# Kernel tuning notes

Hardware: AMD Instinct MI355X
Metric: run time of the kernel (lower is better)

## Reference

```python
import jax, jax.numpy as jnp
import numpy as np

AGENT_THRESH = 0.5
X_DIS_THRESH = 1.5
Y_DIS_THRESH = 3.0
DIS_THRESH = 3.0
LOSS_WEIGHT = 1.0
BIG = 1000000.0

B, A, M, T, C = 128, 2048, 6, 12, 10


def setup_inputs() -> dict:
    key = jax.random.key(0)
    k1, k2, k3, k4, k5 = jax.random.split(key, 5)
    return {
        "ego_fut_preds": jax.random.normal(k1, (B, T, 2), dtype=jnp.float32),
        "agent_preds": jax.random.normal(k2, (B, A, 2), dtype=jnp.float32),
        "agent_fut_preds": jax.random.normal(k3, (B, A, M, T, 2), dtype=jnp.float32),
        "agent_score_preds": jax.random.uniform(k4, (B, A, C), dtype=jnp.float32),
        "agent_fut_cls_preds": jax.random.normal(k5, (B, A, M), dtype=jnp.float32),
    }


def _plan_collision_loss(ego_fut_preds, agent_preds, agent_fut_preds,
                         agent_score_preds, agent_fut_cls_preds):
    # --- invalidate low-score / non-vehicle agents -------------------------
    max_score = jnp.max(agent_score_preds, axis=-1)           # [B, A]
    max_idx = jnp.argmax(agent_score_preds, axis=-1)          # [B, A]
    invalid = (max_score < AGENT_THRESH) | (max_idx > 4)      # [B, A]
    afp = jnp.where(invalid[:, :, None, None, None], BIG, agent_fut_preds)

    # --- select best mode per agent ---------------------------------------
    best_mode = jnp.argmax(agent_fut_cls_preds, axis=-1)      # [B, A]
    afp = jnp.take_along_axis(
        afp, best_mode[:, :, None, None, None], axis=2
    ).squeeze(2)                                              # [B, A, T, 2]

    # --- cumsum deltas -> trajectories -------------------------------------
    pred = jnp.cumsum(ego_fut_preds, axis=-2)                 # [B, T, 2]
    afp = jnp.cumsum(afp, axis=-2)                            # [B, A, T, 2]
    target = agent_preds[:, :, None, :] + afp                 # [B, A, T, 2]

    # --- pairwise distances, far-agent masking -----------------------------
    diff = pred[:, None, :, :] - target                       # [B, A, T, 2]
    dist = jnp.linalg.norm(diff, axis=-1)                     # [B, A, T]
    target = jnp.where((dist > DIS_THRESH)[..., None], BIG, target)

    x_dist = jnp.abs(pred[:, None, :, 0] - target[..., 0])    # [B, A, T]
    y_dist = jnp.abs(pred[:, None, :, 1] - target[..., 1])    # [B, A, T]

    # argmin over agents then gather == min over agents
    x_min = jnp.min(x_dist, axis=1)                           # [B, T]
    y_min = jnp.min(y_dist, axis=1)                           # [B, T]

    x_loss = jnp.where(x_min > X_DIS_THRESH, 0.0, X_DIS_THRESH - x_min)
    y_loss = jnp.where(y_min > Y_DIS_THRESH, 0.0, Y_DIS_THRESH - y_min)
    loss = jnp.stack([x_loss, y_loss], axis=-1)               # [B, T, 2]

    # reduction='mean', weight=None, avg_factor=None
    return LOSS_WEIGHT * jnp.mean(loss)


def reference(ego_fut_preds, agent_preds, agent_fut_preds,
              agent_score_preds, agent_fut_cls_preds):
    return _plan_collision_loss(ego_fut_preds, agent_preds, agent_fut_preds,
                                agent_score_preds, agent_fut_cls_preds)
```

## Files before the change

### kernel.cpp

```cpp
#include <hip/hip_runtime.h>

#define AGENT_THRESH 0.5f
#define X_DIS_THRESH 1.5f
#define Y_DIS_THRESH 3.0f
#define DIS2_THRESH  9.0f
#define LOSS_WEIGHT  1.0f
#define FLT_BIG      3.402823466e+38f

constexpr int B = 128, A = 2048, M = 6, T = 12, C = 10;
constexpr int APB = 256;
constexpr int CHUNKS = A / APB;
constexpr int NBLK = B * CHUNKS;
constexpr int SLOTS = T * 2;
constexpr int GRP = 10;

__global__ __launch_bounds__(APB) void pcl_main_kernel(
    const float* __restrict__ ego,
    const float* __restrict__ agent_preds,
    const float* __restrict__ afp,
    const float* __restrict__ scores,
    const float* __restrict__ cls,
    float* __restrict__ blockmins)
{
    const int b     = blockIdx.x / CHUNKS;
    const int chunk = blockIdx.x % CHUNKS;
    const int tid   = threadIdx.x;
    const int a     = chunk * APB + tid;

    __shared__ float egoraw[SLOTS];
    __shared__ float predx[T], predy[T];
    __shared__ float sred[APB][25];
    __shared__ float spart[SLOTS * GRP];

    const size_t ba = (size_t)b * A + a;

    const float2* sp2 = (const float2*)(scores + ba * C);
    float2 s0 = sp2[0], s1 = sp2[1], s2 = sp2[2], s3 = sp2[3], s4 = sp2[4];
    const float2* cp2 = (const float2*)(cls + ba * M);
    float2 c0 = cp2[0], c1 = cp2[1], c2 = cp2[2];
    const float2 apxy = ((const float2*)agent_preds)[ba];

    if (tid < SLOTS) egoraw[tid] = ego[(size_t)b * SLOTS + tid];
    __syncthreads();
    if (tid == 0) {
        float cx = 0.f, cy = 0.f;
        #pragma unroll
        for (int t = 0; t < T; ++t) {
            cx += egoraw[2 * t + 0];
            cy += egoraw[2 * t + 1];
            predx[t] = cx;
            predy[t] = cy;
        }
    }
    __syncthreads();

    float sv[C] = {s0.x, s0.y, s1.x, s1.y, s2.x, s2.y, s3.x, s3.y, s4.x, s4.y};
    float ms = sv[0];
    int   mi = 0;
    #pragma unroll
    for (int c = 1; c < C; ++c)
        if (sv[c] > ms) { ms = sv[c]; mi = c; }
    const bool valid = (ms >= AGENT_THRESH) && (mi <= 4);

    float p[SLOTS];
    #pragma unroll
    for (int k = 0; k < SLOTS; ++k) p[k] = FLT_BIG;

    if (valid) {
        float cv[M] = {c0.x, c0.y, c1.x, c1.y, c2.x, c2.y};
        float mc = cv[0];
        int   mm = 0;
        #pragma unroll
        for (int m = 1; m < M; ++m)
            if (cv[m] > mc) { mc = cv[m]; mm = m; }

        const float4* fp = (const float4*)(afp + (ba * M + mm) * (size_t)SLOTS);
        float4 f0 = fp[0], f1 = fp[1], f2 = fp[2], f3 = fp[3], f4 = fp[4], f5 = fp[5];
        float dxv[SLOTS];
        dxv[0]=f0.x; dxv[1]=f0.y; dxv[2]=f0.z; dxv[3]=f0.w;
        dxv[4]=f1.x; dxv[5]=f1.y; dxv[6]=f1.z; dxv[7]=f1.w;
        dxv[8]=f2.x; dxv[9]=f2.y; dxv[10]=f2.z; dxv[11]=f2.w;
        dxv[12]=f3.x; dxv[13]=f3.y; dxv[14]=f3.z; dxv[15]=f3.w;
        dxv[16]=f4.x; dxv[17]=f4.y; dxv[18]=f4.z; dxv[19]=f4.w;
        dxv[20]=f5.x; dxv[21]=f5.y; dxv[22]=f5.z; dxv[23]=f5.w;

        float csx = 0.f, csy = 0.f;
        #pragma unroll
        for (int t = 0; t < T; ++t) {
            csx += dxv[2 * t + 0];
            csy += dxv[2 * t + 1];
            const float dx = predx[t] - (apxy.x + csx);
            const float dy = predy[t] - (apxy.y + csy);
            const bool hit = (dx * dx + dy * dy <= DIS2_THRESH);
            p[2 * t + 0] = fminf(p[2 * t + 0], hit ? fabsf(dx) : FLT_BIG);
            p[2 * t + 1] = fminf(p[2 * t + 1], hit ? fabsf(dy) : FLT_BIG);
        }
    }

    #pragma unroll
    for (int k = 0; k < SLOTS; ++k) sred[tid][k] = p[k];
    __syncthreads();

    if (tid < SLOTS * GRP) {
        const int s = tid % SLOTS;
        const int g = tid / SLOTS;
        float pm = FLT_BIG;
        for (int r = g; r < APB; r += GRP) pm = fminf(pm, sred[r][s]);
        spart[tid] = pm;
    }
    __syncthreads();

    if (tid < SLOTS) {
        float m = spart[tid];
        #pragma unroll
        for (int g = 1; g < GRP; ++g) m = fminf(m, spart[g * SLOTS + tid]);
        blockmins[(size_t)blockIdx.x * SLOTS + tid] = m;
    }
}

__global__ __launch_bounds__(256) void pcl_finalize_kernel(
    const float* __restrict__ blockmins, float* __restrict__ out)
{
    float s = 0.f;
    for (int slot = threadIdx.x; slot < B * SLOTS; slot += 256) {
        const int b  = slot / SLOTS;
        const int sc = slot % SLOTS;
        float m = blockmins[((size_t)b * CHUNKS + 0) * SLOTS + sc];
        #pragma unroll
        for (int j = 1; j < CHUNKS; ++j)
            m = fminf(m, blockmins[((size_t)b * CHUNKS + j) * SLOTS + sc]);
        const float thr = (sc & 1) ? Y_DIS_THRESH : X_DIS_THRESH;
        s += (m > thr) ? 0.f : (thr - m);
    }
    #pragma unroll
    for (int off = 32; off > 0; off >>= 1) s += __shfl_down(s, off, 64);
    __shared__ float wsum[4];
    const int wid = threadIdx.x >> 6;
    if ((threadIdx.x & 63) == 0) wsum[wid] = s;
    __syncthreads();
    if (threadIdx.x == 0) {
        float tot = wsum[0] + wsum[1] + wsum[2] + wsum[3];
        out[0] = LOSS_WEIGHT * tot / (float)(B * SLOTS);
    }
}

extern "C" void kernel_launch(void* const* d_in, const int* in_sizes, int n_in,
                              void* d_out, int out_size, void* d_ws, size_t ws_size,
                              hipStream_t stream) {
    const float* ego         = (const float*)d_in[0];
    const float* agent_preds = (const float*)d_in[1];
    const float* afp         = (const float*)d_in[2];
    const float* scores      = (const float*)d_in[3];
    const float* cls         = (const float*)d_in[4];
    float* out               = (float*)d_out;
    float* blockmins         = (float*)d_ws;

    pcl_main_kernel<<<NBLK, APB, 0, stream>>>(
        ego, agent_preds, afp, scores, cls, blockmins);
    pcl_finalize_kernel<<<1, 256, 0, stream>>>(blockmins, out);
}
```

Baseline: 20.14 us.

## Parallelize finalize across batches with last-block atomic reduction

The finalize kernel now runs one block per batch instead of a single block. Each block reduces its chunk minima in shared memory and writes one partial sum, and the last block to arrive (found with an atomic counter) combines all partials. The counter is reset by the main kernel. The ego cumsum prefix is also computed by 24 threads in parallel instead of by one thread. This is meant to cut the serial tail of the single-block finalize, at the cost of an atomic handshake and threadfences.

```diff
diff --git a/kernel.cpp b/kernel.cpp
--- a/kernel.cpp
+++ b/kernel.cpp
@@ -14,18 +14,24 @@
 constexpr int SLOTS = T * 2;
 constexpr int GRP = 10;
 
+constexpr size_t WS_PARTIAL_OFF = (size_t)NBLK * SLOTS;
+constexpr size_t WS_COUNTER_OFF = WS_PARTIAL_OFF + 128;
+
 __global__ __launch_bounds__(APB) void pcl_main_kernel(
     const float* __restrict__ ego,
     const float* __restrict__ agent_preds,
     const float* __restrict__ afp,
     const float* __restrict__ scores,
     const float* __restrict__ cls,
-    float* __restrict__ blockmins)
+    float* __restrict__ blockmins,
+    unsigned int* __restrict__ counter)
 {
     const int b     = blockIdx.x / CHUNKS;
     const int chunk = blockIdx.x % CHUNKS;
     const int tid   = threadIdx.x;
     const int a     = chunk * APB + tid;
+
+    if (blockIdx.x == 0 && tid == 0) *counter = 0;
 
     __shared__ float egoraw[SLOTS];
     __shared__ float predx[T], predy[T];
@@ -42,15 +48,12 @@
 
     if (tid < SLOTS) egoraw[tid] = ego[(size_t)b * SLOTS + tid];
     __syncthreads();
-    if (tid == 0) {
-        float cx = 0.f, cy = 0.f;
-        #pragma unroll
-        for (int t = 0; t < T; ++t) {
-            cx += egoraw[2 * t + 0];
-            cy += egoraw[2 * t + 1];
-            predx[t] = cx;
-            predy[t] = cy;
-        }
+    if (tid < SLOTS) {
+        const int coord = (tid >= T) ? 1 : 0;
+        const int tt    = tid - T * coord;
+        float s = 0.f;
+        for (int i = 0; i <= tt; ++i) s += egoraw[2 * i + coord];
+        if (coord) predy[tt] = s; else predx[tt] = s;
     }
     __syncthreads();
 
@@ -118,29 +121,53 @@
     }
 }
 
-__global__ __launch_bounds__(256) void pcl_finalize_kernel(
-    const float* __restrict__ blockmins, float* __restrict__ out)
+__global__ __launch_bounds__(192) void pcl_finalize_kernel(
+    const float* __restrict__ blockmins,
+    float* __restrict__ partial,
+    unsigned int* __restrict__ counter,
+    float* __restrict__ out)
 {
-    float s = 0.f;
-    for (int slot = threadIdx.x; slot < B * SLOTS; slot += 256) {
-        const int b  = slot / SLOTS;
-        const int sc = slot % SLOTS;
-        float m = blockmins[((size_t)b * CHUNKS + 0) * SLOTS + sc];
+    const int b   = blockIdx.x;
+    const int tid = threadIdx.x;
+
+    __shared__ float sv[CHUNKS * SLOTS];
+    __shared__ float ssum[SLOTS];
+    __shared__ bool  is_last;
+
+    sv[tid] = blockmins[(size_t)b * CHUNKS * SLOTS + tid];
+    __syncthreads();
+
+    if (tid < SLOTS) {
+        float m = sv[tid];
         #pragma unroll
-        for (int j = 1; j < CHUNKS; ++j)
-            m = fminf(m, blockmins[((size_t)b * CHUNKS + j) * SLOTS + sc]);
-        const float thr = (sc & 1) ? Y_DIS_THRESH : X_DIS_THRESH;
-        s += (m > thr) ? 0.f : (thr - m);
+        for (int c = 1; c < CHUNKS; ++c) m = fminf(m, sv[c * SLOTS + tid]);
+        const float thr = (tid & 1) ? Y_DIS_THRESH : X_DIS_THRESH;
+        ssum[tid] = (m > thr) ? 0.f : (thr - m);
     }
-    #pragma unroll
-    for (int off = 32; off > 0; off >>= 1) s += __shfl_down(s, off, 64);
-    __shared__ float wsum[4];
-    const int wid = threadIdx.x >> 6;
-    if ((threadIdx.x & 63) == 0) wsum[wid] = s;
     __syncthreads();
-    if (threadIdx.x == 0) {
-        float tot = wsum[0] + wsum[1] + wsum[2] + wsum[3];
-        out[0] = LOSS_WEIGHT * tot / (float)(B * SLOTS);
+
+    if (tid == 0) {
+        float s = 0.f;
+        #pragma unroll
+        for (int k = 0; k < SLOTS; ++k) s += ssum[k];
+        partial[b] = s;
+        __threadfence();
+        unsigned int prev = atomicAdd(counter, 1u);
+        is_last = (prev == (unsigned int)(B - 1));
+    }
+    __syncthreads();
+
+    if (is_last) {
+        __threadfence();
+        if (tid < 64) {
+            volatile const float* vp = partial;
+            float s = vp[tid] + vp[tid + 64];
+            #pragma unroll
+            for (int off = 32; off > 0; off >>= 1)
+                s += __shfl_down(s, off, 64);
+            if (tid == 0)
+                out[0] = LOSS_WEIGHT * s / (float)(B * SLOTS);
+        }
     }
 }
 
@@ -153,9 +180,12 @@
     const float* scores      = (const float*)d_in[3];
     const float* cls         = (const float*)d_in[4];
     float* out               = (float*)d_out;
+
     float* blockmins         = (float*)d_ws;
+    float* partial           = (float*)d_ws + WS_PARTIAL_OFF;
+    unsigned int* counter    = (unsigned int*)((float*)d_ws + WS_COUNTER_OFF);
 
     pcl_main_kernel<<<NBLK, APB, 0, stream>>>(
-        ego, agent_preds, afp, scores, cls, blockmins);
-    pcl_finalize_kernel<<<1, 256, 0, stream>>>(blockmins, out);
+        ego, agent_preds, afp, scores, cls, blockmins, counter);
+    pcl_finalize_kernel<<<B, 192, 0, stream>>>(blockmins, partial, counter, out);
 }
```

Result: slower. 20.68 us (+2.7%).

## Fuse finalize reduction into main kernel via last-block atomic counter

Applied to the files above, without the earlier changes.

Removes the separate finalize kernel launch: each block bumps a global atomic counter after writing its partial minima, and the block that arrives last does the cross-block min and mean reduction. The counter is never reset and relies on modulo NBLK wrap-around, so it depends on the workspace starting zeroed and persisting across calls. It also parallelizes the ego prefix sum across 24 threads instead of one. The exchange is an atomic plus threadfence per block and one serialized tail block.

```diff
diff --git a/kernel.cpp b/kernel.cpp
--- a/kernel.cpp
+++ b/kernel.cpp
@@ -14,16 +14,19 @@
 constexpr int SLOTS = T * 2;
 constexpr int GRP = 10;
 
-__global__ __launch_bounds__(APB) void pcl_main_kernel(
+__global__ __launch_bounds__(APB) void pcl_fused_kernel(
     const float* __restrict__ ego,
     const float* __restrict__ agent_preds,
     const float* __restrict__ afp,
     const float* __restrict__ scores,
     const float* __restrict__ cls,
-    float* __restrict__ blockmins)
+    float* __restrict__ blockmins,
+    unsigned int* __restrict__ counter,
+    float* __restrict__ out)
 {
-    const int b     = blockIdx.x / CHUNKS;
-    const int chunk = blockIdx.x % CHUNKS;
+    const int bid   = blockIdx.x;
+    const int b     = bid / CHUNKS;
+    const int chunk = bid % CHUNKS;
     const int tid   = threadIdx.x;
     const int a     = chunk * APB + tid;
 
@@ -31,6 +34,8 @@
     __shared__ float predx[T], predy[T];
     __shared__ float sred[APB][25];
     __shared__ float spart[SLOTS * GRP];
+    __shared__ float wsum[4];
+    __shared__ int   slast;
 
     const size_t ba = (size_t)b * A + a;
 
@@ -42,15 +47,12 @@
 
     if (tid < SLOTS) egoraw[tid] = ego[(size_t)b * SLOTS + tid];
     __syncthreads();
-    if (tid == 0) {
-        float cx = 0.f, cy = 0.f;
-        #pragma unroll
-        for (int t = 0; t < T; ++t) {
-            cx += egoraw[2 * t + 0];
-            cy += egoraw[2 * t + 1];
-            predx[t] = cx;
-            predy[t] = cy;
-        }
+    if (tid < SLOTS) {
+        const int coord = (tid >= T) ? 1 : 0;
+        const int tt    = tid - T * coord;
+        float s = 0.f;
+        for (int i = 0; i <= tt; ++i) s += egoraw[2 * i + coord];
+        if (coord) predy[tt] = s; else predx[tt] = s;
     }
     __syncthreads();
 
@@ -114,33 +116,39 @@
         float m = spart[tid];
         #pragma unroll
         for (int g = 1; g < GRP; ++g) m = fminf(m, spart[g * SLOTS + tid]);
-        blockmins[(size_t)blockIdx.x * SLOTS + tid] = m;
+        blockmins[(size_t)bid * SLOTS + tid] = m;
     }
-}
+    __syncthreads();
 
-__global__ __launch_bounds__(256) void pcl_finalize_kernel(
-    const float* __restrict__ blockmins, float* __restrict__ out)
-{
-    float s = 0.f;
-    for (int slot = threadIdx.x; slot < B * SLOTS; slot += 256) {
-        const int b  = slot / SLOTS;
-        const int sc = slot % SLOTS;
-        float m = blockmins[((size_t)b * CHUNKS + 0) * SLOTS + sc];
+    if (tid == 0) {
+        __threadfence();
+        unsigned int prev = atomicAdd(counter, 1u);
+        slast = ((prev % (unsigned)NBLK) == (unsigned)(NBLK - 1)) ? 1 : 0;
+    }
+    __syncthreads();
+
+    if (slast) {
+        __threadfence();
+        volatile const float* vb = blockmins;
+        float s = 0.f;
+        for (int pi = tid; pi < B * SLOTS; pi += APB) {
+            const int bb = pi / SLOTS;
+            const int sl = pi % SLOTS;
+            float m = vb[((size_t)bb * CHUNKS + 0) * SLOTS + sl];
+            #pragma unroll
+            for (int c2 = 1; c2 < CHUNKS; ++c2)
+                m = fminf(m, vb[((size_t)bb * CHUNKS + c2) * SLOTS + sl]);
+            const float thr = (sl & 1) ? Y_DIS_THRESH : X_DIS_THRESH;
+            s += (m > thr) ? 0.f : (thr - m);
+        }
         #pragma unroll
-        for (int j = 1; j < CHUNKS; ++j)
-            m = fminf(m, blockmins[((size_t)b * CHUNKS + j) * SLOTS + sc]);
-        const float thr = (sc & 1) ? Y_DIS_THRESH : X_DIS_THRESH;
-        s += (m > thr) ? 0.f : (thr - m);
-    }
-    #pragma unroll
-    for (int off = 32; off > 0; off >>= 1) s += __shfl_down(s, off, 64);
-    __shared__ float wsum[4];
-    const int wid = threadIdx.x >> 6;
-    if ((threadIdx.x & 63) == 0) wsum[wid] = s;
-    __syncthreads();
-    if (threadIdx.x == 0) {
-        float tot = wsum[0] + wsum[1] + wsum[2] + wsum[3];
-        out[0] = LOSS_WEIGHT * tot / (float)(B * SLOTS);
+        for (int off = 32; off > 0; off >>= 1) s += __shfl_down(s, off, 64);
+        if ((tid & 63) == 0) wsum[tid >> 6] = s;
+        __syncthreads();
+        if (tid == 0) {
+            float tot = wsum[0] + wsum[1] + wsum[2] + wsum[3];
+            out[0] = LOSS_WEIGHT * tot / (float)(B * SLOTS);
+        }
     }
 }
 
@@ -153,9 +161,10 @@
     const float* scores      = (const float*)d_in[3];
     const float* cls         = (const float*)d_in[4];
     float* out               = (float*)d_out;
+
     float* blockmins         = (float*)d_ws;
+    unsigned int* counter    = (unsigned int*)d_ws + NBLK * SLOTS + 32;
 
-    pcl_main_kernel<<<NBLK, APB, 0, stream>>>(
-        ego, agent_preds, afp, scores, cls, blockmins);
-    pcl_finalize_kernel<<<1, 256, 0, stream>>>(blockmins, out);
+    pcl_fused_kernel<<<NBLK, APB, 0, stream>>>(
+        ego, agent_preds, afp, scores, cls, blockmins, counter, out);
 }
```

Result: slower. 51.61 us (+156.3%).
